# Optimization experiments

Hardware: AMD Instinct MI355X
Metric: run time of the kernel (lower is better)

## Reference

```python
import jax, jax.numpy as jnp
import numpy as np

B, S, E = 4, 1024, 1024   # batch, seq_len, emb_dim
H = 8                      # num_head
D = E                      # in_emb_dim defaults to emb_dim
NEG = -9e15                # source uses -9000000000000000.0


def setup_inputs() -> dict:
    key = jax.random.key(0)
    kq, kk, kv, kwq, kwk, kwv, kwl = jax.random.split(key, 7)
    q = jax.random.normal(kq, (B, S, E), dtype=jnp.float32)
    k = jax.random.normal(kk, (B, S, E), dtype=jnp.float32)
    v = jax.random.normal(kv, (B, S, E), dtype=jnp.float32)
    # Per-head Linear(emb_dim -> in_emb_dim, bias=False) weights, torch layout [out, in]
    Wq = jax.random.normal(kwq, (H, D, E), dtype=jnp.float32) * 0.02
    Wk = jax.random.normal(kwk, (H, D, E), dtype=jnp.float32) * 0.02
    Wv = jax.random.normal(kwv, (H, D, E), dtype=jnp.float32) * 0.02
    # last_dense: Linear(in_emb_dim*num_head -> emb_dim, bias=False)
    Wlast = jax.random.normal(kwl, (E, H * D), dtype=jnp.float32) * 0.02
    return {"q": q, "k": k, "v": v, "Wq": Wq, "Wk": Wk, "Wv": Wv, "Wlast": Wlast}


def reference(q, k, v, Wq, Wk, Wv, Wlast):
    # batched per-head projections: y = x @ W[h].T  -> [B,H,S,D]
    in_q = jnp.einsum('bse,hde->bhsd', q, Wq)
    in_k = jnp.einsum('bse,hde->bhsd', k, Wk)
    in_v = jnp.einsum('bse,hde->bhsd', v, Wv)
    # faithful: scaled by sqrt(kv sequence length), not head dim
    scale = 1.0 / jnp.sqrt(jnp.float32(k.shape[-2]))
    logits = jnp.einsum('bhqd,bhkd->bhqk', in_q, in_k) * scale
    # source maps exactly-zero logits to -9e15 before softmax
    logits = jnp.where(logits != 0, logits, jnp.full_like(logits, NEG))
    atten = jax.nn.softmax(logits, axis=-1)          # [B,H,Sq,Sk]
    out_h = jnp.einsum('bhqk,bhkd->bhqd', atten, in_v)
    # concat heads along last dim in head order (matches torch.cat loop)
    b, h, sq, d = out_h.shape
    h_cat = out_h.transpose(0, 2, 1, 3).reshape(b, sq, h * d)
    return jnp.einsum('bsf,ef->bse', h_cat, Wlast)   # last_dense, bias=False
```

## Files before the change

### kernel.cpp

```cpp
#include <hip/hip_runtime.h>
#include <stdint.h>

typedef _Float16 f16;
typedef _Float16 f16x8 __attribute__((ext_vector_type(8)));
typedef _Float16 f16x4 __attribute__((ext_vector_type(4)));
typedef float f32x4 __attribute__((ext_vector_type(4)));

__device__ __forceinline__ void gload_lds16(const void* g, void* l) {
    __builtin_amdgcn_global_load_lds(
        (const __attribute__((address_space(1))) unsigned int*)g,
        (__attribute__((address_space(3))) unsigned int*)l, 16, 0, 0);
}

struct Cvt4 {
    const float* s[4];
    f16* d[4];
    int n8[4];
};
__global__ __launch_bounds__(256) void cvt_plain4(Cvt4 c) {
    const int seg = blockIdx.y;
    const int i = blockIdx.x * 256 + threadIdx.x;
    if (i >= c.n8[seg]) return;
    const float4* s4 = (const float4*)c.s[seg];
    float4 a = s4[2 * (size_t)i];
    float4 b = s4[2 * (size_t)i + 1];
    f16x8 o;
    o[0] = (f16)a.x; o[1] = (f16)a.y; o[2] = (f16)a.z; o[3] = (f16)a.w;
    o[4] = (f16)b.x; o[5] = (f16)b.y; o[6] = (f16)b.z; o[7] = (f16)b.w;
    *(f16x8*)(c.d[seg] + (size_t)i * 8) = o;
}

struct T3 { const float* s[3]; f16* d[3]; };
__global__ __launch_bounds__(256) void cvt_transpose3(T3 c) {
    const int bid = blockIdx.x;
    const int dt = bid & 15;
    const int et = (bid >> 4) & 15;
    const int zz = bid >> 8;
    const int m = zz >> 3, h = zz & 7;
    const float* src = c.s[m] + (size_t)h * 1048576;
    f16* dst = c.d[m] + (size_t)h * 1048576;
    __shared__ f16 t[64][72];
    const int r  = threadIdx.x >> 2;
    const int cq = threadIdx.x & 3;
    const int d0 = dt * 64, e0 = et * 64;
#pragma unroll
    for (int i = 0; i < 4; ++i) {
        const int cc = cq * 4 + i * 16;
        float4 vv = *(const float4*)(src + (size_t)(d0 + r) * 1024 + e0 + cc);
        t[cc + 0][r] = (f16)vv.x;
        t[cc + 1][r] = (f16)vv.y;
        t[cc + 2][r] = (f16)vv.z;
        t[cc + 3][r] = (f16)vv.w;
    }
    __syncthreads();
#pragma unroll
    for (int i = 0; i < 4; ++i) {
        const int cc = cq * 4 + i * 16;
        f16x4 w;
        w[0] = t[r][cc + 0];
        w[1] = t[r][cc + 1];
        w[2] = t[r][cc + 2];
        w[3] = t[r][cc + 3];
        *(f16x4*)(dst + (size_t)(e0 + r) * 1024 + d0 + cc) = w;
    }
}

template <typename OutT>
__global__ __launch_bounds__(256, 2) void gemm_bt(
    const f16* __restrict__ A, const f16* __restrict__ B, OutT* __restrict__ C,
    int ldA, int ldB, long long ldC, int K, float alpha,
    long long sAh, long long sAb, long long sBh, long long sBb,
    long long sCh, long long sCb, int NB) {
    const int z = blockIdx.z;
    const int h = z / NB, bb = z % NB;
    A += h * sAh + bb * sAb;
    B += h * sBh + bb * sBb;
    C += h * sCh + bb * sCb;

    const int row0 = blockIdx.y * 128;
    const int col0 = blockIdx.x * 128;

    __shared__ __align__(16) f16 smA[128 * 64];
    __shared__ __align__(16) f16 smB[128 * 64];

    const int tid  = threadIdx.x;
    const int lane = tid & 63;
    const int wid  = tid >> 6;
    const int wr   = (wid >> 1) * 64;
    const int wc   = (wid & 1) * 64;
    const int fr   = lane & 15;
    const int fkb  = (lane >> 4) * 16;

    f32x4 acc[4][4] = {};

    const int nkt = K >> 6;
    for (int kt = 0; kt < nkt; ++kt) {
#pragma unroll
        for (int it = 0; it < 4; ++it) {
            int p = (it * 256 + tid) * 16;
            int n = p ^ (((p >> 7) & 7) << 4);
            int r   = n >> 7;
            int kel = (n & 127) >> 1;
            size_t ga = (size_t)(row0 + r) * (size_t)ldA + (size_t)(kt * 64 + kel);
            gload_lds16(A + ga, (char*)smA + p);
            size_t gb = (size_t)(col0 + r) * (size_t)ldB + (size_t)(kt * 64 + kel);
            gload_lds16(B + gb, (char*)smB + p);
        }
        __syncthreads();

#pragma unroll
        for (int ks = 0; ks < 2; ++ks) {
            f16x8 af[4], bf[4];
#pragma unroll
            for (int i = 0; i < 4; ++i) {
                int rowA = wr + i * 16 + fr;
                int na   = rowA * 128 + ks * 64 + fkb;
                af[i] = *(const f16x8*)((const char*)smA + (na ^ ((rowA & 7) << 4)));
                int rowB = wc + i * 16 + fr;
                int nb   = rowB * 128 + ks * 64 + fkb;
                bf[i] = *(const f16x8*)((const char*)smB + (nb ^ ((rowB & 7) << 4)));
            }
#pragma unroll
            for (int i = 0; i < 4; ++i)
#pragma unroll
                for (int j = 0; j < 4; ++j)
                    acc[i][j] = __builtin_amdgcn_mfma_f32_16x16x32_f16(
                        af[i], bf[j], acc[i][j], 0, 0, 0);
        }
        __syncthreads();
    }

    const int er = (lane >> 4) * 4;
#pragma unroll
    for (int i = 0; i < 4; ++i)
#pragma unroll
        for (int j = 0; j < 4; ++j)
#pragma unroll
            for (int r = 0; r < 4; ++r) {
                size_t idx = (size_t)(row0 + wr + i * 16 + er + r) * (size_t)ldC +
                             (size_t)(col0 + wc + j * 16 + fr);
                C[idx] = (OutT)(acc[i][j][r] * alpha);
            }
}

__global__ __launch_bounds__(256) void reduce_split2(const float* __restrict__ p,
                                                     float* __restrict__ o, int n4) {
    int i = blockIdx.x * 256 + threadIdx.x;
    if (i >= n4) return;
    const int b  = i >> 18;
    const int jj = i & 262143;
    const float4* p4 = (const float4*)p;
    const size_t base = (size_t)b * 524288 + jj;
    float4 a = p4[base], c = p4[base + 262144];
    float4 s;
    s.x = a.x + c.x;
    s.y = a.y + c.y;
    s.z = a.z + c.z;
    s.w = a.w + c.w;
    ((float4*)o)[i] = s;
}

__global__ __launch_bounds__(256) void softmax_rows(f16* __restrict__ P) {
    const size_t row = blockIdx.x;
    f16* p = P + row * 1024;
    const int tid = threadIdx.x, lane = tid & 63, wid = tid >> 6;

    f16x4 v4 = *(const f16x4*)(p + tid * 4);
    float v[4];
#pragma unroll
    for (int t = 0; t < 4; ++t) {
        v[t] = (float)v4[t];
        if (v[t] == 0.0f) v[t] = -9e15f;
    }
    float m = fmaxf(fmaxf(v[0], v[1]), fmaxf(v[2], v[3]));
#pragma unroll
    for (int o = 32; o > 0; o >>= 1) m = fmaxf(m, __shfl_xor(m, o));
    __shared__ float red[8];
    if (lane == 0) red[wid] = m;
    __syncthreads();
    m = fmaxf(fmaxf(red[0], red[1]), fmaxf(red[2], red[3]));

    float e[4], s = 0.f;
#pragma unroll
    for (int t = 0; t < 4; ++t) { e[t] = __expf(v[t] - m); s += e[t]; }
#pragma unroll
    for (int o = 32; o > 0; o >>= 1) s += __shfl_xor(s, o);
    if (lane == 0) red[4 + wid] = s;
    __syncthreads();
    s = red[4] + red[5] + red[6] + red[7];
    float inv = 1.0f / s;

    f16x4 o4;
#pragma unroll
    for (int t = 0; t < 4; ++t) o4[t] = (f16)(e[t] * inv);
    *(f16x4*)(p + tid * 4) = o4;
}

extern "C" void kernel_launch(void* const* d_in, const int* in_sizes, int n_in,
                              void* d_out, int out_size, void* d_ws, size_t ws_size,
                              hipStream_t stream) {
    const float* q  = (const float*)d_in[0];
    const float* k  = (const float*)d_in[1];
    const float* v  = (const float*)d_in[2];
    const float* Wq = (const float*)d_in[3];
    const float* Wk = (const float*)d_in[4];
    const float* Wv = (const float*)d_in[5];
    const float* Wl = (const float*)d_in[6];
    float* out = (float*)d_out;

    const size_t MB = 1024ull * 1024ull;
    char* ws = (char*)d_ws;
    f16*  q_h  = (f16*)(ws + 0 * MB);
    f16*  k_h  = (f16*)(ws + 8 * MB);
    f16*  v_h  = (f16*)(ws + 16 * MB);
    f16*  Wl_h = (f16*)(ws + 24 * MB);
    f16*  WqT  = (f16*)(ws + 40 * MB);
    f16*  WkT  = (f16*)(ws + 56 * MB);
    f16*  WvT  = (f16*)(ws + 72 * MB);
    f16*  Mt   = (f16*)(ws + 88 * MB);
    f16*  G    = (f16*)(ws + 104 * MB);
    f16*  Aq   = (f16*)(ws + 24 * MB);
    f16*  P    = (f16*)(ws + 120 * MB);
    f16*  Xt   = (f16*)(ws + 24 * MB);
    float* part = (float*)(ws + 88 * MB);

    Cvt4 c4;
    c4.s[0] = q;  c4.d[0] = q_h;  c4.n8[0] = 524288;
    c4.s[1] = k;  c4.d[1] = k_h;  c4.n8[1] = 524288;
    c4.s[2] = v;  c4.d[2] = v_h;  c4.n8[2] = 524288;
    c4.s[3] = Wl; c4.d[3] = Wl_h; c4.n8[3] = 1048576;
    cvt_plain4<<<dim3(4096, 4), 256, 0, stream>>>(c4);

    T3 t3;
    t3.s[0] = Wq; t3.d[0] = WqT;
    t3.s[1] = Wk; t3.d[1] = WkT;
    t3.s[2] = Wv; t3.d[2] = WvT;
    cvt_transpose3<<<6144, 256, 0, stream>>>(t3);

    const long long M1 = 1048576ll;
    const long long M8 = 8388608ll;
    const float SCALE = 0.03125f;
    dim3 blk(256);

    gemm_bt<f16><<<dim3(8, 8, 8), blk, 0, stream>>>(
        WkT, WqT, Mt, 1024, 1024, 1024, 1024, 1.0f,
        M1, 0, M1, 0, M1, 0, 1);
    gemm_bt<f16><<<dim3(8, 8, 8), blk, 0, stream>>>(
        Wl_h, WvT, G, 8192, 1024, 1024, 1024, 1.0f,
        1024, 0, M1, 0, M1, 0, 1);
    gemm_bt<f16><<<dim3(8, 8, 32), blk, 0, stream>>>(
        q_h, Mt, Aq, 1024, 1024, 1024, 1024, 1.0f,
        0, M1, M1, 0, 4 * M1, M1, 4);
    gemm_bt<f16><<<dim3(8, 8, 32), blk, 0, stream>>>(
        Aq, k_h, P, 1024, 1024, 8192, 1024, SCALE,
        4 * M1, M1, 0, M1, 1024, M8, 4);
    gemm_bt<f16><<<dim3(8, 8, 32), blk, 0, stream>>>(
        G, v_h, Xt, 1024, 1024, 8192, 1024, 1.0f,
        M1, 0, 0, M1, 1024, M8, 4);
    softmax_rows<<<32768, 256, 0, stream>>>(P);
    gemm_bt<float><<<dim3(8, 8, 8), blk, 0, stream>>>(
        P, Xt, part, 8192, 8192, 1024, 4096, 1.0f,
        M8, 4096, M8, 4096, 2 * M1, M1, 2);
    reduce_split2<<<4096, 256, 0, stream>>>(part, out, 1048576);
}
```

Measured before the change: 471.5 us.

## Add 256x256-tile double-buffered GEMM with XCD remap for three batched GEMMs

Adds a new GEMM kernel that uses 512-thread workgroups, 256x256 output tiles, direct global-to-LDS loads into double-buffered swizzled LDS, inline ds_read_b128 and MFMA priority scheduling. Workgroups are remapped so consecutive tiles land on the same XCD. The kernel replaces the older 128x128 gemm_bt for the three 32-batch GEMMs (query projection, QK logits, and G·V), aiming for more data reuse per tile and for load latency to overlap compute. It needs 128KB of dynamic LDS and a large accumulator register set, which limits occupancy, and its hand-placed waitcnts and barriers carry correctness risk.

```diff
diff --git a/kernel.cpp b/kernel.cpp
--- a/kernel.cpp
+++ b/kernel.cpp
@@ -11,6 +11,9 @@
         (const __attribute__((address_space(1))) unsigned int*)g,
         (__attribute__((address_space(3))) unsigned int*)l, 16, 0, 0);
 }
+
+#define VMWAIT0() asm volatile("s_waitcnt vmcnt(0)" ::: "memory")
+#define LGKM0()   asm volatile("s_waitcnt lgkmcnt(0)" ::: "memory")
 
 struct Cvt4 {
     const float* s[4];
@@ -143,6 +146,128 @@
             }
 }
 
+template <typename OutT>
+__global__ __launch_bounds__(512, 2) void gemm2ph(
+    const f16* __restrict__ A, const f16* __restrict__ B, OutT* __restrict__ C,
+    int ldA, int ldB, long long ldC, int K, float alpha,
+    long long sAh, long long sAb, long long sBh, long long sBb,
+    long long sCh, long long sCb, int NB, int gx, int gy) {
+    extern __shared__ char lds[];
+
+    const int nwg = gridDim.x;
+    const int q = nwg >> 3, r = nwg & 7;
+    const int xcd = blockIdx.x & 7, lid = blockIdx.x >> 3;
+    const int wg = (xcd < r ? xcd * (q + 1) : r * (q + 1) + (xcd - r) * q) + lid;
+    const int z = wg / (gx * gy);
+    const int rem = wg - z * (gx * gy);
+    const int by = rem / gx, bx = rem - by * gx;
+    const int h = z / NB, bb = z - h * NB;
+    A += h * sAh + bb * sAb;
+    B += h * sBh + bb * sBb;
+    C += h * sCh + bb * sCb;
+    const int row0 = by * 256, col0 = bx * 256;
+
+    const int tid  = threadIdx.x;
+    const int lane = tid & 63;
+    const int wid  = tid >> 6;
+    const int wm   = wid >> 2;
+    const int wn   = wid & 3;
+    const int fr   = lane & 15;
+    const int fkb  = (lane >> 4) << 4;
+    const int sw0  = fkb ^ ((fr & 7) << 4);
+    const int sw1  = sw0 ^ 64;
+
+    const unsigned ldsbase = (unsigned)(uintptr_t)(char*)lds;
+    const unsigned aRow = ldsbase + (unsigned)((wm * 128 + fr) * 128);
+    const unsigned bRow = ldsbase + 32768u + (unsigned)((wn * 64 + fr) * 128);
+
+    const int srow  = tid >> 3;
+    const int scol  = (((tid & 7) ^ ((tid >> 3) & 7)) << 4) >> 1;
+    const f16* gA = A + (size_t)(row0 + srow) * ldA + scol;
+    const f16* gB = B + (size_t)(col0 + srow) * ldB + scol;
+    char* lA = (char*)lds + tid * 16;
+    char* lB = lA + 32768;
+
+    const int nkt = K >> 6;
+
+#define STAGE(tt, bufo) do { \
+        const size_t _ko = (size_t)(tt) * 64; \
+        gload_lds16(gA + _ko,                        lA + (bufo)); \
+        gload_lds16(gA + 64  * (size_t)ldA + _ko,    lA + (bufo) + 8192); \
+        gload_lds16(gA + 128 * (size_t)ldA + _ko,    lA + (bufo) + 16384); \
+        gload_lds16(gA + 192 * (size_t)ldA + _ko,    lA + (bufo) + 24576); \
+        gload_lds16(gB + _ko,                        lB + (bufo)); \
+        gload_lds16(gB + 64  * (size_t)ldB + _ko,    lB + (bufo) + 8192); \
+        gload_lds16(gB + 128 * (size_t)ldB + _ko,    lB + (bufo) + 16384); \
+        gload_lds16(gB + 192 * (size_t)ldB + _ko,    lB + (bufo) + 24576); \
+    } while (0)
+
+#define DSR2(r0, r1, addr, o0, o1) \
+    asm volatile("ds_read_b128 %0, %2 offset:" #o0 "\n\t" \
+                 "ds_read_b128 %1, %2 offset:" #o1 \
+                 : "=&v"(r0), "=&v"(r1) : "v"(addr))
+
+#define MF(i, j, av, bv) \
+    acc[i][j] = __builtin_amdgcn_mfma_f32_16x16x32_f16(av, bv, acc[i][j], 0, 0, 0)
+
+#define HALF(sw) do { \
+        f16x8 a0, a1, a2, a3, a4, a5, a6, a7, b0, b1, b2, b3; \
+        const unsigned aA = aRow + bo + (sw); \
+        const unsigned aB = bRow + bo + (sw); \
+        DSR2(a0, a1, aA, 0, 2048); \
+        DSR2(a2, a3, aA, 4096, 6144); \
+        DSR2(a4, a5, aA, 8192, 10240); \
+        DSR2(a6, a7, aA, 12288, 14336); \
+        DSR2(b0, b1, aB, 0, 2048); \
+        DSR2(b2, b3, aB, 4096, 6144); \
+        LGKM0(); \
+        __builtin_amdgcn_sched_barrier(0); \
+        __builtin_amdgcn_s_setprio(1); \
+        MF(0,0,a0,b0); MF(0,1,a0,b1); MF(0,2,a0,b2); MF(0,3,a0,b3); \
+        MF(1,0,a1,b0); MF(1,1,a1,b1); MF(1,2,a1,b2); MF(1,3,a1,b3); \
+        MF(2,0,a2,b0); MF(2,1,a2,b1); MF(2,2,a2,b2); MF(2,3,a2,b3); \
+        MF(3,0,a3,b0); MF(3,1,a3,b1); MF(3,2,a3,b2); MF(3,3,a3,b3); \
+        MF(4,0,a4,b0); MF(4,1,a4,b1); MF(4,2,a4,b2); MF(4,3,a4,b3); \
+        MF(5,0,a5,b0); MF(5,1,a5,b1); MF(5,2,a5,b2); MF(5,3,a5,b3); \
+        MF(6,0,a6,b0); MF(6,1,a6,b1); MF(6,2,a6,b2); MF(6,3,a6,b3); \
+        MF(7,0,a7,b0); MF(7,1,a7,b1); MF(7,2,a7,b2); MF(7,3,a7,b3); \
+        __builtin_amdgcn_s_setprio(0); \
+    } while (0)
+
+    STAGE(0, 0);
+    VMWAIT0();
+    __builtin_amdgcn_s_barrier();
+
+    f32x4 acc[8][4] = {};
+    unsigned cur = 0;
+
+    for (int t = 0; t < nkt; ++t) {
+        const unsigned bo = cur << 16;
+        if (t + 1 < nkt) STAGE(t + 1, bo ^ 65536u);
+        HALF(sw0);
+        HALF(sw1);
+        VMWAIT0();
+        __builtin_amdgcn_s_barrier();
+        cur ^= 1;
+    }
+#undef HALF
+#undef MF
+#undef DSR2
+#undef STAGE
+
+    const int er = (lane >> 4) * 4;
+#pragma unroll
+    for (int i = 0; i < 8; ++i)
+#pragma unroll
+        for (int j = 0; j < 4; ++j)
+#pragma unroll
+            for (int rr = 0; rr < 4; ++rr) {
+                size_t idx = (size_t)(row0 + wm * 128 + i * 16 + er + rr) * (size_t)ldC +
+                             (size_t)(col0 + wn * 64 + j * 16 + fr);
+                C[idx] = (OutT)(acc[i][j][rr] * alpha);
+            }
+}
+
 __global__ __launch_bounds__(256) void reduce_split2(const float* __restrict__ p,
                                                      float* __restrict__ o, int n4) {
     int i = blockIdx.x * 256 + threadIdx.x;
@@ -208,6 +333,9 @@
     const float* Wl = (const float*)d_in[6];
     float* out = (float*)d_out;
 
+    (void)hipFuncSetAttribute((const void*)gemm2ph<f16>,
+                              hipFuncAttributeMaxDynamicSharedMemorySize, 131072);
+
     const size_t MB = 1024ull * 1024ull;
     char* ws = (char*)d_ws;
     f16*  q_h  = (f16*)(ws + 0 * MB);
@@ -241,6 +369,7 @@
     const long long M8 = 8388608ll;
     const float SCALE = 0.03125f;
     dim3 blk(256);
+    const size_t SMEM = 131072;
 
     gemm_bt<f16><<<dim3(8, 8, 8), blk, 0, stream>>>(
         WkT, WqT, Mt, 1024, 1024, 1024, 1024, 1.0f,
@@ -248,15 +377,15 @@
     gemm_bt<f16><<<dim3(8, 8, 8), blk, 0, stream>>>(
         Wl_h, WvT, G, 8192, 1024, 1024, 1024, 1.0f,
         1024, 0, M1, 0, M1, 0, 1);
-    gemm_bt<f16><<<dim3(8, 8, 32), blk, 0, stream>>>(
+    gemm2ph<f16><<<512, 512, SMEM, stream>>>(
         q_h, Mt, Aq, 1024, 1024, 1024, 1024, 1.0f,
-        0, M1, M1, 0, 4 * M1, M1, 4);
-    gemm_bt<f16><<<dim3(8, 8, 32), blk, 0, stream>>>(
+        0, M1, M1, 0, 4 * M1, M1, 4, 4, 4);
+    gemm2ph<f16><<<512, 512, SMEM, stream>>>(
         Aq, k_h, P, 1024, 1024, 8192, 1024, SCALE,
-        4 * M1, M1, 0, M1, 1024, M8, 4);
-    gemm_bt<f16><<<dim3(8, 8, 32), blk, 0, stream>>>(
+        4 * M1, M1, 0, M1, 1024, M8, 4, 4, 4);
+    gemm2ph<f16><<<512, 512, SMEM, stream>>>(
         G, v_h, Xt, 1024, 1024, 8192, 1024, 1.0f,
-        M1, 0, 0, M1, 1024, M8, 4);
+        M1, 0, 0, M1, 1024, M8, 4, 4, 4);
     softmax_rows<<<32768, 256, 0, stream>>>(P);
     gemm_bt<float><<<dim3(8, 8, 8), blk, 0, stream>>>(
         P, Xt, part, 8192, 8192, 1024, 4096, 1.0f,
```

After: 435.3 us. -7.7%, faster.
